# Performance work log

Measured on AMD Instinct MI355X. Metric: run time of the kernel, lower is better.

## Reference

```python
import jax, jax.numpy as jnp
import numpy as np
from jax import lax

B, T, I, H = 1024, 64, 1024, 1024
EPS = 1e-5


def setup_inputs() -> dict:
    key = jax.random.key(0)
    ks = jax.random.split(key, 12)
    k = 1.0 / np.sqrt(H)  # torch RNNCell init bound
    return {
        "ui": jax.random.randint(ks[0], (B, 8), 0, 10000),
        "uv": jax.random.uniform(ks[1], (B, 8), dtype=jnp.float32),
        "ai": jax.random.randint(ks[2], (B, 8), 0, 10000),
        "av": jax.random.normal(ks[3], (B, T, I), dtype=jnp.float32),
        "y": jax.random.uniform(ks[4], (B, 1), dtype=jnp.float32),
        "W_ih": jax.random.uniform(ks[5], (H, I), minval=-k, maxval=k, dtype=jnp.float32),
        "b_ih": jax.random.uniform(ks[6], (H,), minval=-k, maxval=k, dtype=jnp.float32),
        "W_hh": jax.random.uniform(ks[7], (H, H), minval=-k, maxval=k, dtype=jnp.float32),
        "b_hh": jax.random.uniform(ks[8], (H,), minval=-k, maxval=k, dtype=jnp.float32),
        "W_out": jax.random.uniform(ks[9], (1, H), minval=-k, maxval=k, dtype=jnp.float32),
        "b_out": jax.random.uniform(ks[10], (1,), minval=-k, maxval=k, dtype=jnp.float32),
    }


def reference(ui, uv, ai, av, y, W_ih, b_ih, W_hh, b_hh, W_out, b_out):
    # av: [B, T, I] -> [T, B, I] (matches av.permute([1,0,2]) in source)
    x = jnp.transpose(av, (1, 0, 2))
    h0 = jnp.zeros((av.shape[0], W_hh.shape[0]), dtype=av.dtype)

    def step(h, xt):
        # torch.nn.RNNCell: h' = tanh(x W_ih^T + b_ih + h W_hh^T + b_hh)
        h_new = jnp.tanh(xt @ W_ih.T + b_ih + h @ W_hh.T + b_hh)
        return h_new, None

    h, _ = lax.scan(step, h0, x)
    out = jax.nn.sigmoid(h @ W_out.T + b_out)  # [B, 1]

    # y_true_bool = 1 where y >= 1e-5 else 0
    y_bool = (y >= EPS).astype(out.dtype)
    # torch BCELoss (mean reduction); clamp log like torch does (min -100)
    log_p = jnp.maximum(jnp.log(out), -100.0)
    log_1mp = jnp.maximum(jnp.log1p(-out), -100.0)
    loss = -jnp.mean(y_bool * log_p + (1.0 - y_bool) * log_1mp)
    return loss, out
```

## Files before the change

### kernel.cpp

```cpp
#include <hip/hip_runtime.h>

typedef __attribute__((ext_vector_type(8))) short bf16x8;
typedef __attribute__((ext_vector_type(4))) float f32x4;

__device__ __forceinline__ short f2bf(float f) {
    union { float f; unsigned u; } v; v.f = f;
    unsigned r = v.u + 0x7fffu + ((v.u >> 16) & 1u);
    return (short)(r >> 16);
}
__device__ __forceinline__ float bf2f(short s) {
    union { unsigned u; float f; } v; v.u = ((unsigned)(unsigned short)s) << 16;
    return v.f;
}
__device__ __forceinline__ unsigned pack2(float x, float y) {
    return (unsigned)(unsigned short)f2bf(x) | ((unsigned)(unsigned short)f2bf(y) << 16);
}
__device__ __forceinline__ uint4 pack8(float4 a, float4 b) {
    return make_uint4(pack2(a.x, a.y), pack2(a.z, a.w), pack2(b.x, b.y), pack2(b.z, b.w));
}
__device__ __forceinline__ float tanh_fast(float x) {
    float e = __expf(2.f * x);
    return 1.f - 2.f / (e + 1.f);
}

__device__ __forceinline__ void gll16(const void* gp, void* lp) {
    __builtin_amdgcn_global_load_lds(
        (__attribute__((address_space(1))) void*)gp,
        (__attribute__((address_space(3))) void*)lp, 16, 0, 0);
}

__global__ __launch_bounds__(256) void pack_w(const float* __restrict__ src,
                                              short* __restrict__ dst) {
    int idx = (blockIdx.x * 256 + threadIdx.x) * 8;
    float4 f0 = ((const float4*)(src + idx))[0];
    float4 f1 = ((const float4*)(src + idx))[1];
    *(uint4*)(dst + idx) = pack8(f0, f1);
}

__global__ void prep_b(const float* __restrict__ b_ih, const float* __restrict__ b_hh,
                       float* __restrict__ bsum) {
    int n = threadIdx.x;
    bsum[n] = b_ih[n] + b_hh[n];
}

__global__ __launch_bounds__(256) void conv_av(const float* __restrict__ av,
                                               short* __restrict__ X) {
    size_t e = ((size_t)blockIdx.x * 256 + threadIdx.x) * 8;
    size_t row = e >> 10;
    int k = (int)(e & 1023);
    int b = (int)(row >> 6), t = (int)(row & 63);
    float4 f0 = *(const float4*)(av + e);
    float4 f1 = *(const float4*)(av + e + 4);
    *(uint4*)(X + ((size_t)t * 1024 + b) * 1024 + k) = pack8(f0, f1);
}

__global__ __launch_bounds__(256) void zgemm2(const short* __restrict__ X,
                                              const short* __restrict__ Wih,
                                              const float* __restrict__ bsum,
                                              short* __restrict__ Z) {
    __shared__ short smem[16384];
    short* As = smem;
    short* Bs = smem + 8192;

    const int tid = threadIdx.x, lane = tid & 63, wave = tid >> 6;
    const int wm = wave >> 1, wn = wave & 1;
    const int m0 = blockIdx.y * 128, n0 = blockIdx.x * 128;

    const int srow = wave * 32 + (lane >> 3);
    const int scol = (lane & 7) * 8;
    const short* asrc = X   + (size_t)(m0 + srow) * 1024 + scol;
    const short* bsrc = Wih + (size_t)(n0 + srow) * 1024 + scol;
    char* aldst = (char*)As + wave * 4096;
    char* bldst = (char*)Bs + wave * 4096;

    f32x4 acc[4][4];
    #pragma unroll
    for (int i = 0; i < 4; i++)
        #pragma unroll
        for (int j = 0; j < 4; j++) acc[i][j] = (f32x4)0.0f;

    const int r = lane & 15, q = lane >> 4;
    const int koff = q * 8;

    for (int kt = 0; kt < 16; ++kt) {
        const int kbase = kt * 64;
        #pragma unroll
        for (int i = 0; i < 4; i++) {
            gll16(asrc + kbase + i * 8192, aldst + i * 1024);
            gll16(bsrc + kbase + i * 8192, bldst + i * 1024);
        }
        __syncthreads();

        #pragma unroll
        for (int ks = 0; ks < 2; ++ks) {
            bf16x8 af[4], bfr[4];
            #pragma unroll
            for (int i = 0; i < 4; i++) {
                af[i]  = *(const bf16x8*)&As[(wm * 64 + i * 16 + r) * 64 + ks * 32 + koff];
                bfr[i] = *(const bf16x8*)&Bs[(wn * 64 + i * 16 + r) * 64 + ks * 32 + koff];
            }
            #pragma unroll
            for (int i = 0; i < 4; i++)
                #pragma unroll
                for (int j = 0; j < 4; j++)
                    acc[i][j] = __builtin_amdgcn_mfma_f32_16x16x32_bf16(af[i], bfr[j], acc[i][j], 0, 0, 0);
        }
        __syncthreads();
    }

    short* Csh = smem;
    #pragma unroll
    for (int j = 0; j < 4; j++) {
        int colc = wn * 64 + j * 16 + r;
        float bs = bsum[n0 + colc];
        int chunkc = colc >> 3, rem = colc & 7;
        #pragma unroll
        for (int i = 0; i < 4; i++) {
            int rowb = wm * 64 + i * 16 + q * 4;
            #pragma unroll
            for (int rr = 0; rr < 4; rr++) {
                int row = rowb + rr;
                int sc = ((chunkc ^ (row & 7)) << 3) | rem;
                Csh[row * 128 + sc] = f2bf(acc[i][j][rr] + bs);
            }
        }
    }
    __syncthreads();
    #pragma unroll
    for (int p = 0; p < 8; p++) {
        int row = p * 16 + (tid >> 4);
        int chunk = tid & 15;
        int rc = chunk ^ (row & 7);
        uint4 v = *(const uint4*)&Csh[row * 128 + rc * 8];
        *(uint4*)(Z + (size_t)(m0 + row) * 1024 + n0 + chunk * 8) = v;
    }
}

#define ZLDK 72

__global__ __launch_bounds__(256) void zgemm(const float* __restrict__ av,
                                             const short* __restrict__ Wih,
                                             const float* __restrict__ bsum,
                                             short* __restrict__ Z) {
    __shared__ short As[128 * ZLDK];
    __shared__ short Bs[128 * ZLDK];

    const int tid = threadIdx.x, lane = tid & 63, wave = tid >> 6;
    const int wm = wave >> 1, wn = wave & 1;
    const int m0 = blockIdx.y * 128, n0 = blockIdx.x * 128;
    const int srow = tid >> 1, scol = (tid & 1) * 32;

    const int gr = m0 + srow;
    const int tt = gr >> 10, bb = gr & 1023;
    const float* asrc = av + ((size_t)bb * 64 + tt) * 1024 + scol;
    const short* bsrc = Wih + (size_t)(n0 + srow) * 1024 + scol;

    uint4 ra[4], rb[4];
    #pragma unroll
    for (int j = 0; j < 4; j++) {
        float4 f0 = *(const float4*)(asrc + 8 * j);
        float4 f1 = *(const float4*)(asrc + 8 * j + 4);
        ra[j] = pack8(f0, f1);
        rb[j] = *(const uint4*)(bsrc + 8 * j);
    }

    f32x4 acc[4][4];
    #pragma unroll
    for (int i = 0; i < 4; i++)
        #pragma unroll
        for (int j = 0; j < 4; j++) acc[i][j] = (f32x4)0.0f;

    const int r = lane & 15, q = lane >> 4;
    const int koff = q * 8;

    for (int kt = 0; kt < 16; ++kt) {
        #pragma unroll
        for (int j = 0; j < 4; j++) {
            *(uint4*)&As[srow * ZLDK + scol + 8 * j] = ra[j];
            *(uint4*)&Bs[srow * ZLDK + scol + 8 * j] = rb[j];
        }
        __syncthreads();

        if (kt < 15) {
            int k = (kt + 1) * 64;
            #pragma unroll
            for (int j = 0; j < 4; j++) {
                float4 f0 = *(const float4*)(asrc + k + 8 * j);
                float4 f1 = *(const float4*)(asrc + k + 8 * j + 4);
                ra[j] = pack8(f0, f1);
                rb[j] = *(const uint4*)(bsrc + k + 8 * j);
            }
        }

        #pragma unroll
        for (int ks = 0; ks < 2; ++ks) {
            bf16x8 af[4], bfr[4];
            #pragma unroll
            for (int i = 0; i < 4; i++) {
                af[i]  = *(const bf16x8*)&As[(wm * 64 + i * 16 + r) * ZLDK + ks * 32 + koff];
                bfr[i] = *(const bf16x8*)&Bs[(wn * 64 + i * 16 + r) * ZLDK + ks * 32 + koff];
            }
            #pragma unroll
            for (int i = 0; i < 4; i++)
                #pragma unroll
                for (int j = 0; j < 4; j++)
                    acc[i][j] = __builtin_amdgcn_mfma_f32_16x16x32_bf16(af[i], bfr[j], acc[i][j], 0, 0, 0);
        }
        __syncthreads();
    }

    #pragma unroll
    for (int j = 0; j < 4; j++) {
        int n = n0 + wn * 64 + j * 16 + r;
        float bs = bsum[n];
        #pragma unroll
        for (int i = 0; i < 4; i++) {
            int mb = m0 + wm * 64 + i * 16 + q * 4;
            #pragma unroll
            for (int rr = 0; rr < 4; rr++)
                Z[(size_t)(mb + rr) * 1024 + n] = f2bf(acc[i][j][rr] + bs);
        }
    }
}

__global__ __launch_bounds__(256) void t0_kernel(const short* __restrict__ Z,
                                                 short* __restrict__ h) {
    int idx = (blockIdx.x * 256 + threadIdx.x) * 8;
    uint4 zv = *(const uint4*)(Z + idx);
    const unsigned* zp = (const unsigned*)&zv;
    uint4 out;
    unsigned* op = (unsigned*)&out;
    #pragma unroll
    for (int j = 0; j < 4; j++) {
        float lo = tanh_fast(bf2f((short)(zp[j] & 0xffffu)));
        float hi = tanh_fast(bf2f((short)(zp[j] >> 16)));
        op[j] = pack2(lo, hi);
    }
    *(uint4*)(h + idx) = out;
}

#define SLDK 136

__global__ __launch_bounds__(512) void step_kernel(const short* __restrict__ Whh,
                                                   const short* __restrict__ Z,
                                                   const short* __restrict__ h_in,
                                                   short* __restrict__ h_out, int t) {
    __shared__ short As[64 * SLDK];
    __shared__ short Bs[64 * SLDK];

    const int tid = threadIdx.x, lane = tid & 63, wave = tid >> 6;
    const int wm = wave >> 2, wn = wave & 3;
    const int m0 = blockIdx.y * 64, n0 = blockIdx.x * 64;
    const int srow = tid >> 3, scol = (tid & 7) * 16;

    const short* asrc = h_in + (size_t)(m0 + srow) * 1024 + scol;
    const short* bsrc = Whh + (size_t)(n0 + srow) * 1024 + scol;

    uint4 ra0 = *(const uint4*)asrc;
    uint4 ra1 = *(const uint4*)(asrc + 8);
    uint4 rb0 = *(const uint4*)bsrc;
    uint4 rb1 = *(const uint4*)(bsrc + 8);

    f32x4 acc[2];
    acc[0] = (f32x4)0.0f;
    acc[1] = (f32x4)0.0f;

    const int r = lane & 15, q = lane >> 4;
    const int arow = wm * 32 + r, brow = wn * 16 + r;
    const int koff = q * 8;

    for (int chunk = 0; chunk < 8; ++chunk) {
        *(uint4*)&As[srow * SLDK + scol]     = ra0;
        *(uint4*)&As[srow * SLDK + scol + 8] = ra1;
        *(uint4*)&Bs[srow * SLDK + scol]     = rb0;
        *(uint4*)&Bs[srow * SLDK + scol + 8] = rb1;
        __syncthreads();

        if (chunk < 7) {
            int k = (chunk + 1) * 128;
            ra0 = *(const uint4*)(asrc + k);
            ra1 = *(const uint4*)(asrc + k + 8);
            rb0 = *(const uint4*)(bsrc + k);
            rb1 = *(const uint4*)(bsrc + k + 8);
        }

        #pragma unroll
        for (int ks = 0; ks < 4; ++ks) {
            bf16x8 a0 = *(const bf16x8*)&As[arow * SLDK + ks * 32 + koff];
            bf16x8 a1 = *(const bf16x8*)&As[(arow + 16) * SLDK + ks * 32 + koff];
            bf16x8 b  = *(const bf16x8*)&Bs[brow * SLDK + ks * 32 + koff];
            acc[0] = __builtin_amdgcn_mfma_f32_16x16x32_bf16(a0, b, acc[0], 0, 0, 0);
            acc[1] = __builtin_amdgcn_mfma_f32_16x16x32_bf16(a1, b, acc[1], 0, 0, 0);
        }
        __syncthreads();
    }

    const short* zt = Z + ((size_t)t << 20);
    int n = n0 + wn * 16 + r;
    #pragma unroll
    for (int mi = 0; mi < 2; mi++) {
        int mb = m0 + wm * 32 + mi * 16 + q * 4;
        #pragma unroll
        for (int rr = 0; rr < 4; rr++) {
            float z = bf2f(zt[((size_t)(mb + rr) << 10) + n]);
            h_out[((size_t)(mb + rr) << 10) + n] = f2bf(tanh_fast(acc[mi][rr] + z));
        }
    }
}

__global__ __launch_bounds__(256) void head_kernel(const short* __restrict__ h,
                                                   const float* __restrict__ W_out,
                                                   const float* __restrict__ b_out,
                                                   float* __restrict__ p) {
    int b    = blockIdx.x * 4 + (threadIdx.x >> 6);
    int lane = threadIdx.x & 63;
    float s = 0.f;
    for (int k = lane; k < 1024; k += 64)
        s += bf2f(h[(size_t)b * 1024 + k]) * W_out[k];
    #pragma unroll
    for (int off = 32; off > 0; off >>= 1) s += __shfl_down(s, off);
    if (lane == 0) p[b] = 1.f / (1.f + __expf(-(s + b_out[0])));
}

__global__ __launch_bounds__(1024) void loss_kernel(const float* __restrict__ p,
                                                    const float* __restrict__ y,
                                                    float* __restrict__ loss) {
    __shared__ float red[1024];
    int b = threadIdx.x;
    float pv = p[b];
    float yb = (y[b] >= 1e-5f) ? 1.f : 0.f;
    float lp = fmaxf(logf(pv), -100.f);
    float l1 = fmaxf(log1pf(-pv), -100.f);
    red[b] = yb * lp + (1.f - yb) * l1;
    __syncthreads();
    for (int s = 512; s > 0; s >>= 1) {
        if (b < s) red[b] += red[b + s];
        __syncthreads();
    }
    if (b == 0) loss[0] = -red[0] / 1024.f;
}

extern "C" void kernel_launch(void* const* d_in, const int* in_sizes, int n_in,
                              void* d_out, int out_size, void* d_ws, size_t ws_size,
                              hipStream_t stream) {
    const float* av    = (const float*)d_in[3];
    const float* y     = (const float*)d_in[4];
    const float* W_ih  = (const float*)d_in[5];
    const float* b_ih  = (const float*)d_in[6];
    const float* W_hh  = (const float*)d_in[7];
    const float* b_hh  = (const float*)d_in[8];
    const float* W_out = (const float*)d_in[9];
    const float* b_out = (const float*)d_in[10];
    float* out = (float*)d_out;

    char* ws = (char*)d_ws;
    short* Wih_bf = (short*)ws;
    short* Whh_bf = (short*)(ws + (2u << 20));
    float* bsum   = (float*)(ws + (4u << 20));
    short* hb0    = (short*)(ws + (5u << 20));
    short* hb1    = (short*)(ws + (7u << 20));
    short* Z      = (short*)(ws + (9u << 20));
    short* X      = (short*)(ws + (137u << 20));

    pack_w<<<512, 256, 0, stream>>>(W_ih, Wih_bf);
    pack_w<<<512, 256, 0, stream>>>(W_hh, Whh_bf);
    prep_b<<<1, 1024, 0, stream>>>(b_ih, b_hh, bsum);

    if (ws_size >= ((size_t)266 << 20)) {
        conv_av<<<32768, 256, 0, stream>>>(av, X);
        zgemm2<<<dim3(8, 512), 256, 0, stream>>>(X, Wih_bf, bsum, Z);
    } else {
        zgemm<<<dim3(8, 512), 256, 0, stream>>>(av, Wih_bf, bsum, Z);
    }

    short* hbuf[2] = { hb0, hb1 };
    t0_kernel<<<512, 256, 0, stream>>>(Z, hb1);
    for (int t = 1; t < 64; ++t) {
        short* hin  = hbuf[t & 1];
        short* hout = hbuf[(t + 1) & 1];
        step_kernel<<<dim3(16, 16), 512, 0, stream>>>(Whh_bf, Z, hin, hout, t);
    }
    head_kernel<<<256, 256, 0, stream>>>(hb0, W_out, b_out, out + 1);
    loss_kernel<<<1, 1024, 0, stream>>>(out + 1, y, out);
}
```

Before: 1.272 ms.

## Fuse recurrent steps into persistent cooperative kernel with grid barrier; swizzle zgemm LDS

Replaces the 63 separate step_kernel launches (plus t0) with one cooperative persistent kernel of 256 blocks that loops over timesteps and synchronises with an atomic global barrier. This removes per-step launch overhead and idle gaps between steps. The zgemm2 LDS layout is also XOR-swizzled to reduce bank conflicts on fragment reads. The scan path falls back to the old launches if the cooperative launch fails, and the spin barrier adds a risk of contention or deadlock if the blocks are not all co-resident.

```diff
diff --git a/kernel.cpp b/kernel.cpp
--- a/kernel.cpp
+++ b/kernel.cpp
@@ -22,12 +22,38 @@
     float e = __expf(2.f * x);
     return 1.f - 2.f / (e + 1.f);
 }
+__device__ __forceinline__ uint4 tanh8(uint4 zv) {
+    const unsigned* zp = (const unsigned*)&zv;
+    uint4 out;
+    unsigned* op = (unsigned*)&out;
+    #pragma unroll
+    for (int j = 0; j < 4; j++) {
+        float lo = tanh_fast(bf2f((short)(zp[j] & 0xffffu)));
+        float hi = tanh_fast(bf2f((short)(zp[j] >> 16)));
+        op[j] = pack2(lo, hi);
+    }
+    return out;
+}
 
 __device__ __forceinline__ void gll16(const void* gp, void* lp) {
     __builtin_amdgcn_global_load_lds(
         (__attribute__((address_space(1))) void*)gp,
         (__attribute__((address_space(3))) void*)lp, 16, 0, 0);
 }
+
+__device__ __forceinline__ void gbar(unsigned* bar, unsigned target) {
+    __syncthreads();
+    if (threadIdx.x == 0) {
+        __threadfence();
+        __hip_atomic_fetch_add(bar, 1u, __ATOMIC_RELEASE, __HIP_MEMORY_SCOPE_AGENT);
+        while (__hip_atomic_load(bar, __ATOMIC_ACQUIRE, __HIP_MEMORY_SCOPE_AGENT) < target)
+            __builtin_amdgcn_s_sleep(2);
+    }
+    __syncthreads();
+    __threadfence();
+}
+
+__global__ void zero_bar(unsigned* bar) { *bar = 0; }
 
 __global__ __launch_bounds__(256) void pack_w(const float* __restrict__ src,
                                               short* __restrict__ dst) {
@@ -67,7 +93,7 @@
     const int m0 = blockIdx.y * 128, n0 = blockIdx.x * 128;
 
     const int srow = wave * 32 + (lane >> 3);
-    const int scol = (lane & 7) * 8;
+    const int scol = ((lane & 7) ^ (lane >> 3)) * 8;
     const short* asrc = X   + (size_t)(m0 + srow) * 1024 + scol;
     const short* bsrc = Wih + (size_t)(n0 + srow) * 1024 + scol;
     char* aldst = (char*)As + wave * 4096;
@@ -80,7 +106,6 @@
         for (int j = 0; j < 4; j++) acc[i][j] = (f32x4)0.0f;
 
     const int r = lane & 15, q = lane >> 4;
-    const int koff = q * 8;
 
     for (int kt = 0; kt < 16; ++kt) {
         const int kbase = kt * 64;
@@ -96,8 +121,10 @@
             bf16x8 af[4], bfr[4];
             #pragma unroll
             for (int i = 0; i < 4; i++) {
-                af[i]  = *(const bf16x8*)&As[(wm * 64 + i * 16 + r) * 64 + ks * 32 + koff];
-                bfr[i] = *(const bf16x8*)&Bs[(wn * 64 + i * 16 + r) * 64 + ks * 32 + koff];
+                int ar = wm * 64 + i * 16 + r;
+                int br = wn * 64 + i * 16 + r;
+                af[i]  = *(const bf16x8*)&As[ar * 64 + (((ks * 4 + q) ^ (r & 7)) << 3)];
+                bfr[i] = *(const bf16x8*)&Bs[br * 64 + (((ks * 4 + q) ^ (r & 7)) << 3)];
             }
             #pragma unroll
             for (int i = 0; i < 4; i++)
@@ -226,17 +253,7 @@
 __global__ __launch_bounds__(256) void t0_kernel(const short* __restrict__ Z,
                                                  short* __restrict__ h) {
     int idx = (blockIdx.x * 256 + threadIdx.x) * 8;
-    uint4 zv = *(const uint4*)(Z + idx);
-    const unsigned* zp = (const unsigned*)&zv;
-    uint4 out;
-    unsigned* op = (unsigned*)&out;
-    #pragma unroll
-    for (int j = 0; j < 4; j++) {
-        float lo = tanh_fast(bf2f((short)(zp[j] & 0xffffu)));
-        float hi = tanh_fast(bf2f((short)(zp[j] >> 16)));
-        op[j] = pack2(lo, hi);
-    }
-    *(uint4*)(h + idx) = out;
+    *(uint4*)(h + idx) = tanh8(*(const uint4*)(Z + idx));
 }
 
 #define SLDK 136
@@ -304,6 +321,94 @@
         for (int rr = 0; rr < 4; rr++) {
             float z = bf2f(zt[((size_t)(mb + rr) << 10) + n]);
             h_out[((size_t)(mb + rr) << 10) + n] = f2bf(tanh_fast(acc[mi][rr] + z));
+        }
+    }
+}
+
+#define NBLK 256
+
+__global__ __launch_bounds__(512) void scan_kernel(const short* __restrict__ Whh,
+                                                   const short* __restrict__ Z,
+                                                   short* __restrict__ hA,
+                                                   short* __restrict__ hB,
+                                                   unsigned* __restrict__ bar) {
+    __shared__ short As[64 * SLDK];
+    __shared__ short Bs[64 * SLDK];
+
+    const int tid = threadIdx.x, lane = tid & 63, wave = tid >> 6;
+    const int wm = wave >> 2, wn = wave & 3;
+    const int bid = blockIdx.x;
+    const int m0 = (bid >> 4) * 64, n0 = (bid & 15) * 64;
+
+    {
+        int row = tid >> 3, ch = tid & 7;
+        size_t off = (size_t)(m0 + row) * 1024 + n0 + ch * 8;
+        *(uint4*)(hB + off) = tanh8(*(const uint4*)(Z + off));
+    }
+    unsigned phase = 1;
+    gbar(bar, phase * NBLK);
+
+    const int srow = tid >> 3, scol = (tid & 7) * 16;
+    const int r = lane & 15, q = lane >> 4;
+    const int arow = wm * 32 + r, brow = wn * 16 + r;
+    const int koff = q * 8;
+    const short* bsrc = Whh + (size_t)(n0 + srow) * 1024 + scol;
+
+    for (int t = 1; t < 64; ++t) {
+        const short* h_in  = (t & 1) ? hB : hA;
+        short*       h_out = (t & 1) ? hA : hB;
+        const short* asrc  = h_in + (size_t)(m0 + srow) * 1024 + scol;
+
+        uint4 ra0 = *(const uint4*)asrc;
+        uint4 ra1 = *(const uint4*)(asrc + 8);
+        uint4 rb0 = *(const uint4*)bsrc;
+        uint4 rb1 = *(const uint4*)(bsrc + 8);
+
+        f32x4 acc[2];
+        acc[0] = (f32x4)0.0f;
+        acc[1] = (f32x4)0.0f;
+
+        for (int chunk = 0; chunk < 8; ++chunk) {
+            *(uint4*)&As[srow * SLDK + scol]     = ra0;
+            *(uint4*)&As[srow * SLDK + scol + 8] = ra1;
+            *(uint4*)&Bs[srow * SLDK + scol]     = rb0;
+            *(uint4*)&Bs[srow * SLDK + scol + 8] = rb1;
+            __syncthreads();
+
+            if (chunk < 7) {
+                int k = (chunk + 1) * 128;
+                ra0 = *(const uint4*)(asrc + k);
+                ra1 = *(const uint4*)(asrc + k + 8);
+                rb0 = *(const uint4*)(bsrc + k);
+                rb1 = *(const uint4*)(bsrc + k + 8);
+            }
+
+            #pragma unroll
+            for (int ks = 0; ks < 4; ++ks) {
+                bf16x8 a0 = *(const bf16x8*)&As[arow * SLDK + ks * 32 + koff];
+                bf16x8 a1 = *(const bf16x8*)&As[(arow + 16) * SLDK + ks * 32 + koff];
+                bf16x8 b  = *(const bf16x8*)&Bs[brow * SLDK + ks * 32 + koff];
+                acc[0] = __builtin_amdgcn_mfma_f32_16x16x32_bf16(a0, b, acc[0], 0, 0, 0);
+                acc[1] = __builtin_amdgcn_mfma_f32_16x16x32_bf16(a1, b, acc[1], 0, 0, 0);
+            }
+            __syncthreads();
+        }
+
+        const short* zt = Z + ((size_t)t << 20);
+        int n = n0 + wn * 16 + r;
+        #pragma unroll
+        for (int mi = 0; mi < 2; mi++) {
+            int mb = m0 + wm * 32 + mi * 16 + q * 4;
+            #pragma unroll
+            for (int rr = 0; rr < 4; rr++) {
+                float z = bf2f(zt[((size_t)(mb + rr) << 10) + n]);
+                h_out[((size_t)(mb + rr) << 10) + n] = f2bf(tanh_fast(acc[mi][rr] + z));
+            }
+        }
+
+        if (t < 63) {
+            ++phase;
+            gbar(bar, phase * NBLK);
         }
     }
 }
@@ -357,6 +462,7 @@
     short* Wih_bf = (short*)ws;
     short* Whh_bf = (short*)(ws + (2u << 20));
     float* bsum   = (float*)(ws + (4u << 20));
+    unsigned* bar = (unsigned*)(ws + (4u << 20) + 65536);
     short* hb0    = (short*)(ws + (5u << 20));
     short* hb1    = (short*)(ws + (7u << 20));
     short* Z      = (short*)(ws + (9u << 20));
@@ -365,21 +471,33 @@
     pack_w<<<512, 256, 0, stream>>>(W_ih, Wih_bf);
     pack_w<<<512, 256, 0, stream>>>(W_hh, Whh_bf);
     prep_b<<<1, 1024, 0, stream>>>(b_ih, b_hh, bsum);
-
-    if (ws_size >= ((size_t)266 << 20)) {
+    zero_bar<<<1, 1, 0, stream>>>(bar);
+
+    bool bigws = ws_size >= ((size_t)266 << 20);
+
+    if (bigws) {
         conv_av<<<32768, 256, 0, stream>>>(av, X);
         zgemm2<<<dim3(8, 512), 256, 0, stream>>>(X, Wih_bf, bsum, Z);
     } else {
         zgemm<<<dim3(8, 512), 256, 0, stream>>>(av, Wih_bf, bsum, Z);
     }
 
-    short* hbuf[2] = { hb0, hb1 };
-    t0_kernel<<<512, 256, 0, stream>>>(Z, hb1);
-    for (int t = 1; t < 64; ++t) {
-        short* hin  = hbuf[t & 1];
-        short* hout = hbuf[(t + 1) & 1];
-        step_kernel<<<dim3(16, 16), 512, 0, stream>>>(Whh_bf, Z, hin, hout, t);
-    }
+    bool scanned = false;
+    if (bigws) {
+        const short* a0 = Whh_bf; const short* a1 = Z;
+        short* a2 = hb0; short* a3 = hb1; unsigned* a4 = bar;
+        void* args[5] = { (void*)&a0, (void*)&a1, (void*)&a2, (void*)&a3, (void*)&a4 };
+        hipError_t ce = hipLaunchCooperativeKernel((const void*)scan_kernel,
+                                                   dim3(NBLK), dim3(512), args, 0, stream);
+        scanned = (ce == hipSuccess);
+    }
+    if (!scanned) {
+        short* hbuf[2] = { hb0, hb1 };
+        t0_kernel<<<512, 256, 0, stream>>>(Z, hb1);
+        for (int t = 1; t < 64; ++t)
+            step_kernel<<<dim3(16, 16), 512, 0, stream>>>(Whh_bf, Z, hbuf[t & 1], hbuf[(t + 1) & 1], t);
+    }
+
     head_kernel<<<256, 256, 0, stream>>>(hb0, W_out, b_out, out + 1);
     loss_kernel<<<1, 1024, 0, stream>>>(out + 1, y, out);
 }
```

New measurement: 4.875 ms. 3.83x slower.

## Fuse recurrent timesteps into persistent batch-partitioned scan kernel with swizzled LDS

Applied to the files above, without the earlier changes.

Replaces the 63 per-timestep step_kernel launches with one persistent bscan kernel. Each block owns 16 batch rows and keeps their hidden state in double-buffered LDS for all timesteps, so h never round-trips through global memory and there is no launch per step. Each step streams the full W_hh from global/L2 into registers. Only 64 blocks run, which leaves most CUs idle. Separately, zgemm2 gets an XOR swizzle on its LDS layout to cut bank conflicts.

```diff
diff --git a/kernel.cpp b/kernel.cpp
--- a/kernel.cpp
+++ b/kernel.cpp
@@ -21,6 +21,18 @@
 __device__ __forceinline__ float tanh_fast(float x) {
     float e = __expf(2.f * x);
     return 1.f - 2.f / (e + 1.f);
+}
+__device__ __forceinline__ uint4 tanh8(uint4 zv) {
+    const unsigned* zp = (const unsigned*)&zv;
+    uint4 out;
+    unsigned* op = (unsigned*)&out;
+    #pragma unroll
+    for (int j = 0; j < 4; j++) {
+        float lo = tanh_fast(bf2f((short)(zp[j] & 0xffffu)));
+        float hi = tanh_fast(bf2f((short)(zp[j] >> 16)));
+        op[j] = pack2(lo, hi);
+    }
+    return out;
 }
 
 __device__ __forceinline__ void gll16(const void* gp, void* lp) {
@@ -67,7 +79,7 @@
     const int m0 = blockIdx.y * 128, n0 = blockIdx.x * 128;
 
     const int srow = wave * 32 + (lane >> 3);
-    const int scol = (lane & 7) * 8;
+    const int scol = ((lane & 7) ^ (lane >> 3)) * 8;
     const short* asrc = X   + (size_t)(m0 + srow) * 1024 + scol;
     const short* bsrc = Wih + (size_t)(n0 + srow) * 1024 + scol;
     char* aldst = (char*)As + wave * 4096;
@@ -80,7 +92,6 @@
         for (int j = 0; j < 4; j++) acc[i][j] = (f32x4)0.0f;
 
     const int r = lane & 15, q = lane >> 4;
-    const int koff = q * 8;
 
     for (int kt = 0; kt < 16; ++kt) {
         const int kbase = kt * 64;
@@ -96,8 +107,10 @@
             bf16x8 af[4], bfr[4];
             #pragma unroll
             for (int i = 0; i < 4; i++) {
-                af[i]  = *(const bf16x8*)&As[(wm * 64 + i * 16 + r) * 64 + ks * 32 + koff];
-                bfr[i] = *(const bf16x8*)&Bs[(wn * 64 + i * 16 + r) * 64 + ks * 32 + koff];
+                int ar = wm * 64 + i * 16 + r;
+                int br = wn * 64 + i * 16 + r;
+                af[i]  = *(const bf16x8*)&As[ar * 64 + (((ks * 4 + q) ^ (r & 7)) << 3)];
+                bfr[i] = *(const bf16x8*)&Bs[br * 64 + (((ks * 4 + q) ^ (r & 7)) << 3)];
             }
             #pragma unroll
             for (int i = 0; i < 4; i++)
@@ -226,17 +239,7 @@
 __global__ __launch_bounds__(256) void t0_kernel(const short* __restrict__ Z,
                                                  short* __restrict__ h) {
     int idx = (blockIdx.x * 256 + threadIdx.x) * 8;
-    uint4 zv = *(const uint4*)(Z + idx);
-    const unsigned* zp = (const unsigned*)&zv;
-    uint4 out;
-    unsigned* op = (unsigned*)&out;
-    #pragma unroll
-    for (int j = 0; j < 4; j++) {
-        float lo = tanh_fast(bf2f((short)(zp[j] & 0xffffu)));
-        float hi = tanh_fast(bf2f((short)(zp[j] >> 16)));
-        op[j] = pack2(lo, hi);
-    }
-    *(uint4*)(h + idx) = out;
+    *(uint4*)(h + idx) = tanh8(*(const uint4*)(Z + idx));
 }
 
 #define SLDK 136
@@ -305,6 +308,107 @@
             float z = bf2f(zt[((size_t)(mb + rr) << 10) + n]);
             h_out[((size_t)(mb + rr) << 10) + n] = f2bf(tanh_fast(acc[mi][rr] + z));
         }
+    }
+}
+
+__global__ __launch_bounds__(1024) void bscan(const short* __restrict__ Whh,
+                                              const short* __restrict__ Z,
+                                              short* __restrict__ hout) {
+    __shared__ short Ad[2][16 * 1024];
+    __shared__ short Zs[16 * 1032];
+
+    const int tid = threadIdx.x, lane = tid & 63, wave = tid >> 6;
+    const int m0 = blockIdx.x * 16;
+    const int r = lane & 15, q = lane >> 4;
+    const int nbase = wave * 64;
+
+    const int zrow = tid >> 6;
+    const int zc0 = (tid & 63) * 2;
+
+    const short* wp0 = Whh + (size_t)(nbase +  0 + r) * 1024 + q * 8;
+    const short* wp1 = Whh + (size_t)(nbase + 16 + r) * 1024 + q * 8;
+    const short* wp2 = Whh + (size_t)(nbase + 32 + r) * 1024 + q * 8;
+    const short* wp3 = Whh + (size_t)(nbase + 48 + r) * 1024 + q * 8;
+
+    {
+        const short* z0 = Z + (size_t)(m0 + zrow) * 1024 + zc0 * 8;
+        uint4 v0 = tanh8(*(const uint4*)z0);
+        uint4 v1 = tanh8(*(const uint4*)(z0 + 8));
+        *(uint4*)&Ad[0][zrow * 1024 + ((zc0 ^ (zrow & 7)) << 3)]       = v0;
+        *(uint4*)&Ad[0][zrow * 1024 + (((zc0 + 1) ^ (zrow & 7)) << 3)] = v1;
+    }
+    __syncthreads();
+
+    int cur = 0;
+    for (int t = 1; t < 64; ++t) {
+        const short* zt = Z + ((size_t)t << 20) + (size_t)(m0 + zrow) * 1024 + zc0 * 8;
+        uint4 zv0 = *(const uint4*)zt;
+        uint4 zv1 = *(const uint4*)(zt + 8);
+
+        f32x4 acc[4];
+        acc[0] = (f32x4)0.0f; acc[1] = (f32x4)0.0f;
+        acc[2] = (f32x4)0.0f; acc[3] = (f32x4)0.0f;
+
+        const short* ab = &Ad[cur][0];
+
+        uint4 b0[4], b1[4];
+        b0[0] = *(const uint4*)wp0; b0[1] = *(const uint4*)wp1;
+        b0[2] = *(const uint4*)wp2; b0[3] = *(const uint4*)wp3;
+
+        for (int kc = 0; kc < 32; kc += 2) {
+            b1[0] = *(const uint4*)(wp0 + (kc + 1) * 32);
+            b1[1] = *(const uint4*)(wp1 + (kc + 1) * 32);
+            b1[2] = *(const uint4*)(wp2 + (kc + 1) * 32);
+            b1[3] = *(const uint4*)(wp3 + (kc + 1) * 32);
+
+            bf16x8 a0 = *(const bf16x8*)&ab[r * 1024 + (((kc * 4 + q) ^ (r & 7)) << 3)];
+            acc[0] = __builtin_amdgcn_mfma_f32_16x16x32_bf16(a0, *(const bf16x8*)&b0[0], acc[0], 0, 0, 0);
+            acc[1] = __builtin_amdgcn_mfma_f32_16x16x32_bf16(a0, *(const bf16x8*)&b0[1], acc[1], 0, 0, 0);
+            acc[2] = __builtin_amdgcn_mfma_f32_16x16x32_bf16(a0, *(const bf16x8*)&b0[2], acc[2], 0, 0, 0);
+            acc[3] = __builtin_amdgcn_mfma_f32_16x16x32_bf16(a0, *(const bf16x8*)&b0[3], acc[3], 0, 0, 0);
+
+            if (kc + 2 < 32) {
+                b0[0] = *(const uint4*)(wp0 + (kc + 2) * 32);
+                b0[1] = *(const uint4*)(wp1 + (kc + 2) * 32);
+                b0[2] = *(const uint4*)(wp2 + (kc + 2) * 32);
+                b0[3] = *(const uint4*)(wp3 + (kc + 2) * 32);
+            }
+
+            bf16x8 a1 = *(const bf16x8*)&ab[r * 1024 + ((((kc + 1) * 4 + q) ^ (r & 7)) << 3)];
+            acc[0] = __builtin_amdgcn_mfma_f32_16x16x32_bf16(a1, *(const bf16x8*)&b1[0], acc[0], 0, 0, 0);
+            acc[1] = __builtin_amdgcn_mfma_f32_16x16x32_bf16(a1, *(const bf16x8*)&b1[1], acc[1], 0, 0, 0);
+            acc[2] = __builtin_amdgcn_mfma_f32_16x16x32_bf16(a1, *(const bf16x8*)&b1[2], acc[2], 0, 0, 0);
+            acc[3] = __builtin_amdgcn_mfma_f32_16x16x32_bf16(a1, *(const bf16x8*)&b1[3], acc[3], 0, 0, 0);
+        }
+
+        *(uint4*)&Zs[zrow * 1032 + zc0 * 8]     = zv0;
+        *(uint4*)&Zs[zrow * 1032 + zc0 * 8 + 8] = zv1;
+        __syncthreads();
+
+        const int nxt = cur ^ 1;
+        #pragma unroll
+        for (int nf = 0; nf < 4; nf++) {
+            int col = nbase + nf * 16 + r;
+            int cc = col >> 3, rem = col & 7;
+            #pragma unroll
+            for (int rr = 0; rr < 4; rr++) {
+                int row = q * 4 + rr;
+                float z = bf2f(Zs[row * 1032 + col]);
+                Ad[nxt][row * 1024 + ((cc ^ (row & 7)) << 3) + rem] =
+                    f2bf(tanh_fast(acc[nf][rr] + z));
+            }
+        }
+        __syncthreads();
+        cur = nxt;
+    }
+
+    {
+        const short* fin = &Ad[cur][0];
+        uint4 v0 = *(const uint4*)&fin[zrow * 1024 + ((zc0 ^ (zrow & 7)) << 3)];
+        uint4 v1 = *(const uint4*)&fin[zrow * 1024 + (((zc0 + 1) ^ (zrow & 7)) << 3)];
+        short* dst = hout + (size_t)(m0 + zrow) * 1024 + zc0 * 8;
+        *(uint4*)dst = v0;
+        *(uint4*)(dst + 8) = v1;
     }
 }
 
@@ -366,20 +470,20 @@
     pack_w<<<512, 256, 0, stream>>>(W_hh, Whh_bf);
     prep_b<<<1, 1024, 0, stream>>>(b_ih, b_hh, bsum);
 
-    if (ws_size >= ((size_t)266 << 20)) {
+    bool bigws = ws_size >= ((size_t)266 << 20);
+
+    if (bigws) {
         conv_av<<<32768, 256, 0, stream>>>(av, X);
         zgemm2<<<dim3(8, 512), 256, 0, stream>>>(X, Wih_bf, bsum, Z);
+        bscan<<<64, 1024, 0, stream>>>(Whh_bf, Z, hb0);
     } else {
         zgemm<<<dim3(8, 512), 256, 0, stream>>>(av, Wih_bf, bsum, Z);
-    }
-
-    short* hbuf[2] = { hb0, hb1 };
-    t0_kernel<<<512, 256, 0, stream>>>(Z, hb1);
-    for (int t = 1; t < 64; ++t) {
-        short* hin  = hbuf[t & 1];
-        short* hout = hbuf[(t + 1) & 1];
-        step_kernel<<<dim3(16, 16), 512, 0, stream>>>(Whh_bf, Z, hin, hout, t);
-    }
+        short* hbuf[2] = { hb0, hb1 };
+        t0_kernel<<<512, 256, 0, stream>>>(Z, hb1);
+        for (int t = 1; t < 64; ++t)
+            step_kernel<<<dim3(16, 16), 512, 0, stream>>>(Whh_bf, Z, hbuf[t & 1], hbuf[(t + 1) & 1], t);
+    }
+
     head_kernel<<<256, 256, 0, stream>>>(hb0, W_out, b_out, out + 1);
     loss_kernel<<<1, 1024, 0, stream>>>(out + 1, y, out);
 }
```

New measurement: 4.134 ms. 3.25x slower.

## Restructure recurrent step kernel, swizzle LDS and remap input GEMM blocks

Applied to the files above, without the earlier changes.

The per-timestep kernel is rewritten so each block stages a full 32x1024 slice of h in swizzled LDS through global_load_lds. W_hh fragments are then streamed straight from global memory into MFMA, with no K-chunked LDS loop and its repeated barriers. The Z tile is prefetched into LDS, and output goes through a swizzled LDS buffer so h_out stores are coalesced. The input-projection GEMM gets an XOR-swizzled LDS layout to avoid bank conflicts and a 1D grid remap for better L2 locality. Reading W_hh directly from global relies on L2 hits, and the larger LDS footprint may limit occupancy.

```diff
diff --git a/kernel.cpp b/kernel.cpp
--- a/kernel.cpp
+++ b/kernel.cpp
@@ -21,6 +21,18 @@
 __device__ __forceinline__ float tanh_fast(float x) {
     float e = __expf(2.f * x);
     return 1.f - 2.f / (e + 1.f);
+}
+__device__ __forceinline__ uint4 tanh8(uint4 zv) {
+    const unsigned* zp = (const unsigned*)&zv;
+    uint4 out;
+    unsigned* op = (unsigned*)&out;
+    #pragma unroll
+    for (int j = 0; j < 4; j++) {
+        float lo = tanh_fast(bf2f((short)(zp[j] & 0xffffu)));
+        float hi = tanh_fast(bf2f((short)(zp[j] >> 16)));
+        op[j] = pack2(lo, hi);
+    }
+    return out;
 }
 
 __device__ __forceinline__ void gll16(const void* gp, void* lp) {
@@ -64,10 +76,14 @@
 
     const int tid = threadIdx.x, lane = tid & 63, wave = tid >> 6;
     const int wm = wave >> 1, wn = wave & 1;
-    const int m0 = blockIdx.y * 128, n0 = blockIdx.x * 128;
+    const int pid = blockIdx.x;
+    const int slot = pid >> 3;
+    const int mt = (pid & 7) * 64 + (slot >> 3);
+    const int nt = slot & 7;
+    const int m0 = mt * 128, n0 = nt * 128;
 
     const int srow = wave * 32 + (lane >> 3);
-    const int scol = (lane & 7) * 8;
+    const int scol = ((lane & 7) ^ (lane >> 3)) * 8;
     const short* asrc = X   + (size_t)(m0 + srow) * 1024 + scol;
     const short* bsrc = Wih + (size_t)(n0 + srow) * 1024 + scol;
     char* aldst = (char*)As + wave * 4096;
@@ -80,7 +96,6 @@
         for (int j = 0; j < 4; j++) acc[i][j] = (f32x4)0.0f;
 
     const int r = lane & 15, q = lane >> 4;
-    const int koff = q * 8;
 
     for (int kt = 0; kt < 16; ++kt) {
         const int kbase = kt * 64;
@@ -96,8 +111,10 @@
             bf16x8 af[4], bfr[4];
             #pragma unroll
             for (int i = 0; i < 4; i++) {
-                af[i]  = *(const bf16x8*)&As[(wm * 64 + i * 16 + r) * 64 + ks * 32 + koff];
-                bfr[i] = *(const bf16x8*)&Bs[(wn * 64 + i * 16 + r) * 64 + ks * 32 + koff];
+                int ar = wm * 64 + i * 16 + r;
+                int br = wn * 64 + i * 16 + r;
+                af[i]  = *(const bf16x8*)&As[ar * 64 + (((ks * 4 + q) ^ (r & 7)) << 3)];
+                bfr[i] = *(const bf16x8*)&Bs[br * 64 + (((ks * 4 + q) ^ (r & 7)) << 3)];
             }
             #pragma unroll
             for (int i = 0; i < 4; i++)
@@ -226,85 +243,69 @@
 __global__ __launch_bounds__(256) void t0_kernel(const short* __restrict__ Z,
                                                  short* __restrict__ h) {
     int idx = (blockIdx.x * 256 + threadIdx.x) * 8;
-    uint4 zv = *(const uint4*)(Z + idx);
-    const unsigned* zp = (const unsigned*)&zv;
-    uint4 out;
-    unsigned* op = (unsigned*)&out;
-    #pragma unroll
-    for (int j = 0; j < 4; j++) {
-        float lo = tanh_fast(bf2f((short)(zp[j] & 0xffffu)));
-        float hi = tanh_fast(bf2f((short)(zp[j] >> 16)));
-        op[j] = pack2(lo, hi);
-    }
-    *(uint4*)(h + idx) = out;
-}
-
-#define SLDK 136
-
-__global__ __launch_bounds__(512) void step_kernel(const short* __restrict__ Whh,
-                                                   const short* __restrict__ Z,
-                                                   const short* __restrict__ h_in,
-                                                   short* __restrict__ h_out, int t) {
-    __shared__ short As[64 * SLDK];
-    __shared__ short Bs[64 * SLDK];
+    *(uint4*)(h + idx) = tanh8(*(const uint4*)(Z + idx));
+}
+
+__global__ __launch_bounds__(512) void step2(const short* __restrict__ Whh,
+                                             const short* __restrict__ Z,
+                                             const short* __restrict__ h_in,
+                                             short* __restrict__ h_out, int t) {
+    __shared__ short As[32 * 1024];
+    __shared__ short Zs[32 * 128];
+    __shared__ short Csh[32 * 128];
 
     const int tid = threadIdx.x, lane = tid & 63, wave = tid >> 6;
-    const int wm = wave >> 2, wn = wave & 3;
-    const int m0 = blockIdx.y * 64, n0 = blockIdx.x * 64;
-    const int srow = tid >> 3, scol = (tid & 7) * 16;
-
-    const short* asrc = h_in + (size_t)(m0 + srow) * 1024 + scol;
-    const short* bsrc = Whh + (size_t)(n0 + srow) * 1024 + scol;
-
-    uint4 ra0 = *(const uint4*)asrc;
-    uint4 ra1 = *(const uint4*)(asrc + 8);
-    uint4 rb0 = *(const uint4*)bsrc;
-    uint4 rb1 = *(const uint4*)(bsrc + 8);
-
-    f32x4 acc[2];
-    acc[0] = (f32x4)0.0f;
-    acc[1] = (f32x4)0.0f;
-
+    const int m0 = blockIdx.y * 32, n0 = blockIdx.x * 128;
     const int r = lane & 15, q = lane >> 4;
-    const int arow = wm * 32 + r, brow = wn * 16 + r;
-    const int koff = q * 8;
-
-    for (int chunk = 0; chunk < 8; ++chunk) {
-        *(uint4*)&As[srow * SLDK + scol]     = ra0;
-        *(uint4*)&As[srow * SLDK + scol + 8] = ra1;
-        *(uint4*)&Bs[srow * SLDK + scol]     = rb0;
-        *(uint4*)&Bs[srow * SLDK + scol + 8] = rb1;
-        __syncthreads();
-
-        if (chunk < 7) {
-            int k = (chunk + 1) * 128;
-            ra0 = *(const uint4*)(asrc + k);
-            ra1 = *(const uint4*)(asrc + k + 8);
-            rb0 = *(const uint4*)(bsrc + k);
-            rb1 = *(const uint4*)(bsrc + k + 8);
-        }
-
-        #pragma unroll
-        for (int ks = 0; ks < 4; ++ks) {
-            bf16x8 a0 = *(const bf16x8*)&As[arow * SLDK + ks * 32 + koff];
-            bf16x8 a1 = *(const bf16x8*)&As[(arow + 16) * SLDK + ks * 32 + koff];
-            bf16x8 b  = *(const bf16x8*)&Bs[brow * SLDK + ks * 32 + koff];
-            acc[0] = __builtin_amdgcn_mfma_f32_16x16x32_bf16(a0, b, acc[0], 0, 0, 0);
-            acc[1] = __builtin_amdgcn_mfma_f32_16x16x32_bf16(a1, b, acc[1], 0, 0, 0);
-        }
-        __syncthreads();
-    }
-
-    const short* zt = Z + ((size_t)t << 20);
-    int n = n0 + wn * 16 + r;
+
+    #pragma unroll
+    for (int i = 0; i < 8; i++) {
+        int j = wave * 8 + i;
+        int R = j >> 1, half = j & 1;
+        const short* src = h_in + (size_t)(m0 + R) * 1024 + half * 512
+                         + ((lane ^ (R & 7)) << 3);
+        gll16(src, (char*)As + j * 1024);
+    }
+    {
+        const short* src = Z + ((size_t)t << 20)
+                         + (size_t)(m0 + wave * 4 + (lane >> 4)) * 1024
+                         + n0 + ((lane & 15) << 3);
+        gll16(src, (char*)Zs + wave * 1024);
+    }
+    __syncthreads();
+
+    const short* wp = Whh + (size_t)(n0 + wave * 16 + r) * 1024 + q * 8;
+    const int axor = r & 7;
+    f32x4 acc0 = (f32x4)0.0f, acc1 = (f32x4)0.0f;
+
+    #pragma unroll 8
+    for (int ks = 0; ks < 32; ++ks) {
+        int co = ((ks * 4 + q) ^ axor) << 3;
+        bf16x8 a0 = *(const bf16x8*)&As[r * 1024 + co];
+        bf16x8 a1 = *(const bf16x8*)&As[(16 + r) * 1024 + co];
+        bf16x8 b  = *(const bf16x8*)(wp + ks * 32);
+        acc0 = __builtin_amdgcn_mfma_f32_16x16x32_bf16(a0, b, acc0, 0, 0, 0);
+        acc1 = __builtin_amdgcn_mfma_f32_16x16x32_bf16(a1, b, acc1, 0, 0, 0);
+    }
+
+    const int col = wave * 16 + r;
+    const int cc = col >> 3, rem = col & 7;
     #pragma unroll
     for (int mi = 0; mi < 2; mi++) {
-        int mb = m0 + wm * 32 + mi * 16 + q * 4;
+        const f32x4 a = mi ? acc1 : acc0;
         #pragma unroll
         for (int rr = 0; rr < 4; rr++) {
-            float z = bf2f(zt[((size_t)(mb + rr) << 10) + n]);
-            h_out[((size_t)(mb + rr) << 10) + n] = f2bf(tanh_fast(acc[mi][rr] + z));
-        }
+            int row = mi * 16 + q * 4 + rr;
+            float z = bf2f(Zs[row * 128 + col]);
+            Csh[row * 128 + ((cc ^ (row & 7)) << 3) + rem] = f2bf(tanh_fast(a[rr] + z));
+        }
+    }
+    __syncthreads();
+    {
+        int row = tid >> 4, chunk = tid & 15;
+        int rc = chunk ^ (row & 7);
+        uint4 v = *(const uint4*)&Csh[row * 128 + rc * 8];
+        *(uint4*)(h_out + (size_t)(m0 + row) * 1024 + n0 + chunk * 8) = v;
     }
 }
 
@@ -366,20 +367,20 @@
     pack_w<<<512, 256, 0, stream>>>(W_hh, Whh_bf);
     prep_b<<<1, 1024, 0, stream>>>(b_ih, b_hh, bsum);
 
-    if (ws_size >= ((size_t)266 << 20)) {
+    bool bigws = ws_size >= ((size_t)266 << 20);
+
+    if (bigws) {
         conv_av<<<32768, 256, 0, stream>>>(av, X);
-        zgemm2<<<dim3(8, 512), 256, 0, stream>>>(X, Wih_bf, bsum, Z);
+        zgemm2<<<4096, 256, 0, stream>>>(X, Wih_bf, bsum, Z);
     } else {
         zgemm<<<dim3(8, 512), 256, 0, stream>>>(av, Wih_bf, bsum, Z);
     }
 
     short* hbuf[2] = { hb0, hb1 };
     t0_kernel<<<512, 256, 0, stream>>>(Z, hb1);
-    for (int t = 1; t < 64; ++t) {
-        short* hin  = hbuf[t & 1];
-        short* hout = hbuf[(t + 1) & 1];
-        step_kernel<<<dim3(16, 16), 512, 0, stream>>>(Whh_bf, Z, hin, hout, t);
-    }
+    for (int t = 1; t < 64; ++t)
+        step2<<<dim3(8, 32), 512, 0, stream>>>(Whh_bf, Z, hbuf[t & 1], hbuf[(t + 1) & 1], t);
+
     head_kernel<<<256, 256, 0, stream>>>(hb0, W_out, b_out, out + 1);
     loss_kernel<<<1, 1024, 0, stream>>>(out + 1, y, out);
 }
```

Result: slower. 1.452 ms (+14.2%).
